# Kernel optimization log

Hardware: AMD Instinct MI355X
Metric: run time of the kernel (lower is better)

The kernel has to match this reference:

```python
import jax, jax.numpy as jnp
import numpy as np

N = 32768
E = 8           # num_submodules (4x2 grid)
HID = 256       # hidden_dim
POS_DIM = 63    # 3*(1+2*10)
DIR_DIM = 27    # 3*(1+2*4)
APP_DIM = 48
IN_DIM = POS_DIM + APP_DIM        # 111
SKIP_IN = HID + IN_DIM            # 367
COL_IN = HID + DIR_DIM            # 283
COL_HID = HID // 2                # 128
NUM_APP = 1000

SCENE = np.array([-100.0, -100.0, -10.0, 100.0, 100.0, 50.0], np.float32)
_margin = (1.0 - 0.8) / 2.0       # (1 - foreground_ratio)/2
_rng = SCENE[3:] - SCENE[:3]
FG_LO = SCENE[:3] + _rng * _margin
FG_HI = SCENE[3:] - _rng * _margin

def _centroids():
    xs = np.linspace(-100.0, 100.0, 3)   # grid_cols + 1
    ys = np.linspace(-100.0, 100.0, 5)   # grid_rows + 1
    zc = (-10.0 + 50.0) / 2.0
    cs = []
    for i in range(4):
        for j in range(2):
            cs.append([(xs[j] + xs[j + 1]) / 2.0, (ys[i] + ys[i + 1]) / 2.0, zc])
    return np.asarray(cs, np.float32)
CENTROIDS = _centroids()  # [E,3]

def posenc(x, max_log2, num_freqs):
    freqs = (2.0 ** np.linspace(0.0, max_log2, num_freqs)).astype(np.float32)
    parts = [x]
    for f in freqs:
        parts.append(jnp.sin(f * x))
        parts.append(jnp.cos(f * x))
    return jnp.concatenate(parts, axis=-1)

def setup_inputs() -> dict:
    key = jax.random.key(0)
    ks = jax.random.split(key, 24)
    lo, hi = jnp.asarray(SCENE[:3]), jnp.asarray(SCENE[3:])
    points = jax.random.uniform(ks[0], (N, 3), jnp.float32) * (hi - lo) + lo
    vd = jax.random.normal(ks[1], (N, 3), jnp.float32)
    viewdirs = vd / jnp.linalg.norm(vd, axis=-1, keepdims=True)
    appearance_idx = jax.random.randint(ks[2], (N,), 0, NUM_APP, jnp.int32)
    s = 0.02
    p = lambda k, shape: jax.random.normal(k, shape, jnp.float32) * s
    return {
        'points': points, 'viewdirs': viewdirs, 'appearance_idx': appearance_idx,
        'app_embed': p(ks[3], (E, NUM_APP, APP_DIM)),
        'W0': p(ks[4], (E, IN_DIM, HID)),      'b0': p(ks[5], (E, HID)),
        'W_pre': p(ks[6], (E, 3, HID, HID)),   'b_pre': p(ks[7], (E, 3, HID)),
        'Wskip': p(ks[8], (E, SKIP_IN, HID)),  'bskip': p(ks[9], (E, HID)),
        'W_post': p(ks[10], (E, 3, HID, HID)), 'b_post': p(ks[11], (E, 3, HID)),
        'Wd': p(ks[12], (E, HID, 1)),          'bd': p(ks[13], (E, 1)),
        'Wf': p(ks[14], (E, HID, HID)),        'bf': p(ks[15], (E, HID)),
        'Wc1': p(ks[16], (E, COL_IN, COL_HID)),'bc1': p(ks[17], (E, COL_HID)),
        'Wc2': p(ks[18], (E, COL_HID, 3)),     'bc2': p(ks[19], (E, 3)),
    }

def _forward(points, viewdirs, appearance_idx, app_embed, W0, b0, W_pre, b_pre,
             Wskip, bskip, W_post, b_post, Wd, bd, Wf, bf, Wc1, bc1, Wc2, bc2):
    n = points.shape[0]
    cen = jnp.asarray(CENTROIDS)
    fg = jnp.all((points >= jnp.asarray(FG_LO)) & (points <= jnp.asarray(FG_HI)), axis=-1)  # [N]
    # nearest-centroid routing (argmin of L2 == argmin of squared L2)
    expert = jnp.argmin(jnp.sum((points[:, None, :] - cen[None]) ** 2, axis=-1), axis=1)  # [N]
    pe = posenc(points, 10.0, 10)                              # [N,63]
    app = app_embed[:, appearance_idx, :]                      # [E,N,48] per-expert embedding lookup
    x0 = jnp.concatenate([jnp.broadcast_to(pe[None], (E, n, POS_DIM)), app], axis=-1)  # [E,N,111]
    x = jax.nn.relu(jnp.einsum('eni,eih->enh', x0, W0) + b0[:, None])
    for i in range(3):  # linear layers 1..3
        x = jax.nn.relu(jnp.einsum('enh,ehk->enk', x, W_pre[:, i]) + b_pre[:, i][:, None])
    x = jnp.concatenate([x, x0], axis=-1)                      # skip connection at layer 4
    x = jax.nn.relu(jnp.einsum('eni,eih->enh', x, Wskip) + bskip[:, None])
    for i in range(3):  # linear layers 5..7
        x = jax.nn.relu(jnp.einsum('enh,ehk->enk', x, W_post[:, i]) + b_post[:, i][:, None])
    density = jax.nn.relu(jnp.einsum('enh,eho->eno', x, Wd) + bd[:, None])   # [E,N,1]
    feat = jnp.einsum('enh,ehk->enk', x, Wf) + bf[:, None]                   # feature_head (no relu)
    de = posenc(viewdirs, 4.0, 4)                              # [N,27]
    cin = jnp.concatenate([feat, jnp.broadcast_to(de[None], (E, n, DIR_DIM))], axis=-1)  # [E,N,283]
    h = jax.nn.relu(jnp.einsum('eni,eih->enh', cin, Wc1) + bc1[:, None])
    color = jax.nn.sigmoid(jnp.einsum('enh,eho->eno', h, Wc2) + bc2[:, None])  # [E,N,3]
    rows = jnp.arange(n)
    d = jnp.where(fg[:, None], density[expert, rows], 0.0)     # combine: pick routed expert, zero bg
    c = jnp.where(fg[:, None], color[expert, rows], 0.0)
    return d, c

def reference(points, viewdirs, appearance_idx, app_embed, W0, b0, W_pre, b_pre,
              Wskip, bskip, W_post, b_post, Wd, bd, Wf, bf, Wc1, bc1, Wc2, bc2):
    return _forward(points, viewdirs, appearance_idx, app_embed, W0, b0, W_pre, b_pre,
                    Wskip, bskip, W_post, b_post, Wd, bd, Wf, bf, Wc1, bc1, Wc2, bc2)
```

## Files before the change

### kernel.cpp

```cpp
#include <hip/hip_runtime.h>
#include <hip/hip_bf16.h>
#include <math.h>

typedef __bf16 bf16;
typedef __bf16 bf16x4 __attribute__((ext_vector_type(4)));
typedef __bf16 bf16x8 __attribute__((ext_vector_type(8)));
typedef float  f32x4  __attribute__((ext_vector_type(4)));

#define N_PTS 32768

__global__ void k_point(const float* __restrict__ pts, float* __restrict__ out,
                        int* __restrict__ counts, unsigned short* __restrict__ idxlist) {
    __shared__ int lcnt[8], lbase[8];
    int t = threadIdx.x;
    int n = blockIdx.x * 256 + t;
    if (t < 8) lcnt[t] = 0;
    __syncthreads();
    float px = pts[3*n+0], py = pts[3*n+1], pz = pts[3*n+2];
    int e = 0; float best = 3.4e38f;
    #pragma unroll
    for (int i = 0; i < 4; ++i)
        #pragma unroll
        for (int j = 0; j < 2; ++j) {
            float cx = j ? 50.f : -50.f, cy = -75.f + 50.f * i;
            float dx = px - cx, dy = py - cy, dz = pz - 20.f;
            float d = dx*dx + dy*dy + dz*dz;
            if (d < best) { best = d; e = i*2 + j; }
        }
    bool fg = (px >= -80.f && px <= 80.f && py >= -80.f && py <= 80.f &&
               pz >= -4.f  && pz <= 44.f);
    int slot = -1;
    if (fg) {
        slot = atomicAdd(&lcnt[e], 1);
    } else {
        out[n] = 0.f;
        out[N_PTS + 3*n + 0] = 0.f;
        out[N_PTS + 3*n + 1] = 0.f;
        out[N_PTS + 3*n + 2] = 0.f;
    }
    __syncthreads();
    if (t < 8) lbase[t] = atomicAdd(&counts[t], lcnt[t]);
    __syncthreads();
    if (slot >= 0) idxlist[e * N_PTS + lbase[e] + slot] = (unsigned short)n;
}

__global__ void k_tp(const float* __restrict__ s0, const float* __restrict__ s1,
                     const float* __restrict__ s2, const float* __restrict__ s3,
                     const float* __restrict__ s4, const float* __restrict__ s5,
                     bf16* __restrict__ d0, bf16* __restrict__ d1, bf16* __restrict__ d2,
                     bf16* __restrict__ d3, bf16* __restrict__ d4, bf16* __restrict__ d5,
                     const float* __restrict__ pts, float* __restrict__ out,
                     int* __restrict__ counts, unsigned short* __restrict__ idxlist) {
    int t = threadIdx.x;
    if (blockIdx.y == 6) {
        __shared__ int lcnt[8], lbase[8];
        if (blockIdx.x >= N_PTS / 256) return;
        int n = blockIdx.x * 256 + t;
        if (t < 8) lcnt[t] = 0;
        __syncthreads();
        float px = pts[3*n+0], py = pts[3*n+1], pz = pts[3*n+2];
        int e = 0; float best = 3.4e38f;
        #pragma unroll
        for (int i = 0; i < 4; ++i)
            #pragma unroll
            for (int j = 0; j < 2; ++j) {
                float cx = j ? 50.f : -50.f, cy = -75.f + 50.f * i;
                float dx = px - cx, dy = py - cy, dz = pz - 20.f;
                float d = dx*dx + dy*dy + dz*dz;
                if (d < best) { best = d; e = i*2 + j; }
            }
        bool fg = (px >= -80.f && px <= 80.f && py >= -80.f && py <= 80.f &&
                   pz >= -4.f  && pz <= 44.f);
        int slot = -1;
        if (fg) {
            slot = atomicAdd(&lcnt[e], 1);
        } else {
            out[n] = 0.f;
            out[N_PTS + 3*n + 0] = 0.f;
            out[N_PTS + 3*n + 1] = 0.f;
            out[N_PTS + 3*n + 2] = 0.f;
        }
        __syncthreads();
        if (t < 8) lbase[t] = atomicAdd(&counts[t], lcnt[t]);
        __syncthreads();
        if (slot >= 0) idxlist[e * N_PTS + lbase[e] + slot] = (unsigned short)n;
        return;
    }
    __shared__ bf16 tile[64 * 68];
    const float* src; bf16* dst; int K, Nn, Kpad, Eg;
    switch (blockIdx.y) {
        case 0:  src = s0; dst = d0; K = 111; Nn = 256; Kpad = 128; Eg = 8;  break;
        case 1:  src = s1; dst = d1; K = 256; Nn = 256; Kpad = 256; Eg = 24; break;
        case 2:  src = s2; dst = d2; K = 367; Nn = 256; Kpad = 384; Eg = 8;  break;
        case 3:  src = s3; dst = d3; K = 256; Nn = 256; Kpad = 256; Eg = 24; break;
        case 4:  src = s4; dst = d4; K = 256; Nn = 256; Kpad = 256; Eg = 8;  break;
        default: src = s5; dst = d5; K = 283; Nn = 128; Kpad = 288; Eg = 8;  break;
    }
    int ktiles = (Kpad + 63) / 64, ntiles = Nn / 64;
    int b = blockIdx.x;
    if (b >= Eg * ktiles * ntiles) return;
    int eg = b / (ktiles * ntiles), rem = b % (ktiles * ntiles);
    int kt = rem / ntiles, nt = rem % ntiles;
    #pragma unroll
    for (int r = 0; r < 4; ++r) {
        int idx = r * 256 + t;
        int kl = idx >> 4, nl4 = (idx & 15) * 4;
        int kg = kt * 64 + kl, ng = nt * 64 + nl4;
        bf16x4 v = (bf16x4){(bf16)0.f, (bf16)0.f, (bf16)0.f, (bf16)0.f};
        if (kg < K) {
            f32x4 f = *(const f32x4*)(src + ((size_t)(eg * K + kg)) * Nn + ng);
            v[0] = (bf16)f[0]; v[1] = (bf16)f[1]; v[2] = (bf16)f[2]; v[3] = (bf16)f[3];
        }
        *(bf16x4*)(&tile[kl * 68 + nl4]) = v;
    }
    __syncthreads();
    #pragma unroll
    for (int i = 0; i < 2; ++i) {
        int idx = i * 256 + t;
        int ng_l = idx >> 3, kq = idx & 7;
        int kg = kt * 64 + kq * 8, ng = nt * 64 + ng_l;
        if (kg < Kpad) {
            bf16x8 v;
            #pragma unroll
            for (int j = 0; j < 8; ++j) v[j] = tile[(kq * 8 + j) * 68 + ng_l];
            size_t off = ((size_t)(ng >> 5) * (Kpad >> 5) + (size_t)(kg >> 5)) * 1024
                       + (size_t)((ng >> 4) & 1) * 512
                       + (size_t)((kg >> 3) & 3) * 128
                       + (size_t)(ng & 15) * 8;
            *(bf16x8*)(dst + (size_t)eg * Nn * Kpad + off) = v;
        }
    }
}

__device__ __forceinline__ f32x4 mfma16(bf16x8 a, bf16x8 b, f32x4 c) {
    return __builtin_amdgcn_mfma_f32_16x16x32_bf16(a, b, c, 0, 0, 0);
}

__device__ __forceinline__ void zacc(f32x4 acc[2][2]) {
    #pragma unroll
    for (int i = 0; i < 2; ++i)
        #pragma unroll
        for (int j = 0; j < 2; ++j) acc[i][j] = (f32x4){0.f, 0.f, 0.f, 0.f};
}

template<int NS, int KPAD>
__device__ __forceinline__ void gemm_p(f32x4 acc[2][2], const bf16* A, int astr,
                                       const bf16* __restrict__ Wt, int wk0,
                                       int nbase, int l16, int quad, int lane) {
    const bf16* bp = Wt + ((size_t)(nbase >> 5) * (KPAD >> 5) + (size_t)(wk0 >> 5)) * 1024
                   + (size_t)lane * 8;
    #pragma unroll
    for (int s = 0; s < NS; ++s) {
        int kA = s * 32 + quad * 8;
        bf16x8 a0 = *(const bf16x8*)(A + (size_t)(l16)      * astr + kA);
        bf16x8 a1 = *(const bf16x8*)(A + (size_t)(16 + l16) * astr + kA);
        bf16x8 b0 = *(const bf16x8*)(bp + s * 1024);
        bf16x8 b1 = *(const bf16x8*)(bp + s * 1024 + 512);
        acc[0][0] = mfma16(a0, b0, acc[0][0]);
        acc[1][0] = mfma16(a1, b0, acc[1][0]);
        acc[0][1] = mfma16(a0, b1, acc[0][1]);
        acc[1][1] = mfma16(a1, b1, acc[1][1]);
    }
}

template<int NS, bool GUARD>
__device__ __forceinline__ void gemm_g(f32x4 acc[2][2], const bf16* A, int astr,
                                       const float* __restrict__ W, int ldn, int wk0, int Klim,
                                       int nbase, int l16, int quad) {
    #pragma unroll
    for (int s = 0; s < NS; ++s) {
        int kA = s * 32 + quad * 8;
        bf16x8 a0 = *(const bf16x8*)(A + (size_t)(l16)      * astr + kA);
        bf16x8 a1 = *(const bf16x8*)(A + (size_t)(16 + l16) * astr + kA);
        #pragma unroll
        for (int nt = 0; nt < 2; ++nt) {
            int n = nbase + nt * 16 + l16;
            const float* wp = W + (size_t)(wk0 + kA) * ldn + n;
            bf16x8 b;
            #pragma unroll
            for (int j = 0; j < 8; ++j) {
                float wv = 0.f;
                if (!GUARD || (wk0 + kA + j < Klim)) wv = wp[(size_t)j * ldn];
                b[j] = (bf16)wv;
            }
            acc[0][nt] = mfma16(a0, b, acc[0][nt]);
            acc[1][nt] = mfma16(a1, b, acc[1][nt]);
        }
    }
}

__device__ __forceinline__ void epi(f32x4 acc[2][2], const float* bias, bool dorelu,
                                    bf16* dst, int dstr, int nbase, int l16, int quad) {
    #pragma unroll
    for (int nt = 0; nt < 2; ++nt) {
        float bv = bias[nbase + nt * 16 + l16];
        #pragma unroll
        for (int mt = 0; mt < 2; ++mt) {
            #pragma unroll
            for (int r = 0; r < 4; ++r) {
                float v = acc[mt][nt][r] + bv;
                v = fminf(fmaxf(v, -64.f), 64.f);
                if (dorelu) v = fmaxf(v, 0.f);
                dst[(size_t)(mt * 16 + quad * 4 + r) * dstr + nbase + nt * 16 + l16] = (bf16)v;
            }
        }
    }
}

template<bool PACKED>
__global__ __launch_bounds__(512, 2)
void k_main(const int* __restrict__ counts, const unsigned short* __restrict__ idxlist,
            const float* __restrict__ pts, const float* __restrict__ dirs,
            const float* __restrict__ app_embed, const int* __restrict__ aidx,
            const float* __restrict__ W0, const float* __restrict__ b0,
            const float* __restrict__ W_pre, const float* __restrict__ b_pre,
            const float* __restrict__ Wskip, const float* __restrict__ bskip,
            const float* __restrict__ W_post, const float* __restrict__ b_post,
            const float* __restrict__ Wd, const float* __restrict__ bd,
            const float* __restrict__ Wf, const float* __restrict__ bf_,
            const float* __restrict__ Wc1, const float* __restrict__ bc1,
            const float* __restrict__ Wc2, const float* __restrict__ bc2,
            const bf16* __restrict__ wt0, const bf16* __restrict__ wtpre,
            const bf16* __restrict__ wtskip, const bf16* __restrict__ wtpost,
            const bf16* __restrict__ wtf, const bf16* __restrict__ wtc1,
            float* __restrict__ out) {
    __shared__ bf16 xaA[32 * 264];
    __shared__ bf16 xaB[32 * 264];
    __shared__ bf16 x0l[32 * 136];
    __shared__ bf16 del[32 * 48];
    __shared__ int  gidx[32];
    __shared__ int  aid[32];

    const int e    = blockIdx.x & 7;
    const int tile = blockIdx.x >> 3;
    const int cnt  = counts[e];
    if (tile * 32 >= cnt) return;
    const int t = threadIdx.x;
    const int lane = t & 63, wv = t >> 6;
    const int l16 = lane & 15, quad = lane >> 4;
    const int nbase = wv * 32;

    if (t < 32) {
        int i = tile * 32 + t;
        int g = (i < cnt) ? (int)idxlist[e * N_PTS + i] : -1;
        gidx[t] = g;
        aid[t]  = (g >= 0) ? aidx[g] : 0;
    }
    __syncthreads();
    {
        int row = t >> 4, c0 = t & 15, g = gidx[row];
        float p0 = 0.f, p1 = 0.f, p2 = 0.f, q0 = 0.f, q1 = 0.f, q2 = 0.f;
        if (g >= 0) {
            p0 = pts[3*g+0];  p1 = pts[3*g+1];  p2 = pts[3*g+2];
            q0 = dirs[3*g+0]; q1 = dirs[3*g+1]; q2 = dirs[3*g+2];
        }
        int ai = aid[row];
        #pragma unroll
        for (int i = 0; i < 8; ++i) {
            int col = c0 + 16 * i;
            float v = 0.f;
            if (g >= 0 && col < 111) {
                if (col < 3) {
                    v = (col == 0) ? p0 : (col == 1) ? p1 : p2;
                } else if (col < 63) {
                    int q = col - 3, fi = q / 6, d = q % 6, ax = (d < 3) ? d : (d - 3);
                    float p = (ax == 0) ? p0 : (ax == 1) ? p1 : p2;
                    float f = (float)exp2((double)fi * (10.0 / 9.0));
                    v = (d < 3) ? sinf(f * p) : cosf(f * p);
                } else {
                    v = app_embed[((size_t)(e * 1000 + ai)) * 48 + (col - 63)];
                }
            }
            x0l[row * 136 + col] = (bf16)v;
        }
        #pragma unroll
        for (int i = 0; i < 2; ++i) {
            int col = c0 + 16 * i;
            float v = 0.f;
            if (g >= 0 && col < 27) {
                if (col < 3) {
                    v = (col == 0) ? q0 : (col == 1) ? q1 : q2;
                } else {
                    int q = col - 3, fi = q / 6, d = q % 6, ax = (d < 3) ? d : (d - 3);
                    float p = (ax == 0) ? q0 : (ax == 1) ? q1 : q2;
                    float f = (float)exp2((double)fi * (4.0 / 3.0));
                    v = (d < 3) ? sinf(f * p) : cosf(f * p);
                }
            }
            del[row * 48 + col] = (bf16)v;
        }
    }
    __syncthreads();

    f32x4 acc[2][2];
    zacc(acc);
    if (PACKED) gemm_p<4, 128>(acc, x0l, 136, wt0 + (size_t)e * 32768, 0, nbase, l16, quad, lane);
    else        gemm_g<4, true>(acc, x0l, 136, W0 + (size_t)e * 28416, 256, 0, 111, nbase, l16, quad);
    epi(acc, b0 + e * 256, true, xaA, 264, nbase, l16, quad);
    __syncthreads();
    #pragma unroll
    for (int i = 0; i < 3; ++i) {
        const bf16* src = (i & 1) ? xaB : xaA;
        bf16*       dst = (i & 1) ? xaA : xaB;
        zacc(acc);
        if (PACKED) gemm_p<8, 256>(acc, src, 264, wtpre + (size_t)(e * 3 + i) * 65536, 0, nbase, l16, quad, lane);
        else        gemm_g<8, false>(acc, src, 264, W_pre + (size_t)(e * 3 + i) * 65536, 256, 0, 256, nbase, l16, quad);
        epi(acc, b_pre + (e * 3 + i) * 256, true, dst, 264, nbase, l16, quad);
        __syncthreads();
    }
    zacc(acc);
    if (PACKED) {
        gemm_p<8, 384>(acc, xaB, 264, wtskip + (size_t)e * 98304, 0,   nbase, l16, quad, lane);
        gemm_p<4, 384>(acc, x0l, 136, wtskip + (size_t)e * 98304, 256, nbase, l16, quad, lane);
    } else {
        gemm_g<8, false>(acc, xaB, 264, Wskip + (size_t)e * 93952, 256, 0,   367, nbase, l16, quad);
        gemm_g<4, true >(acc, x0l, 136, Wskip + (size_t)e * 93952, 256, 256, 367, nbase, l16, quad);
    }
    epi(acc, bskip + e * 256, true, xaA, 264, nbase, l16, quad);
    __syncthreads();
    #pragma unroll
    for (int i = 0; i < 3; ++i) {
        const bf16* src = (i & 1) ? xaB : xaA;
        bf16*       dst = (i & 1) ? xaA : xaB;
        zacc(acc);
        if (PACKED) gemm_p<8, 256>(acc, src, 264, wtpost + (size_t)(e * 3 + i) * 65536, 0, nbase, l16, quad, lane);
        else        gemm_g<8, false>(acc, src, 264, W_post + (size_t)(e * 3 + i) * 65536, 256, 0, 256, nbase, l16, quad);
        epi(acc, b_post + (e * 3 + i) * 256, true, dst, 264, nbase, l16, quad);
        __syncthreads();
    }
    {
        int m = t >> 4, p = t & 15;
        const bf16*  xr = xaB + (size_t)m * 264;
        const float* wd = Wd + e * 256;
        float s = 0.f;
        #pragma unroll
        for (int kk = 0; kk < 16; ++kk) s += (float)xr[p * 16 + kk] * wd[p * 16 + kk];
        s += __shfl_down(s, 8, 16);
        s += __shfl_down(s, 4, 16);
        s += __shfl_down(s, 2, 16);
        s += __shfl_down(s, 1, 16);
        if (p == 0) {
            int g = gidx[m];
            if (g >= 0) out[g] = fminf(fmaxf(s + bd[e], 0.f), 64.f);
        }
    }
    zacc(acc);
    if (PACKED) gemm_p<8, 256>(acc, xaB, 264, wtf + (size_t)e * 65536, 0, nbase, l16, quad, lane);
    else        gemm_g<8, false>(acc, xaB, 264, Wf + (size_t)e * 65536, 256, 0, 256, nbase, l16, quad);
    epi(acc, bf_ + e * 256, false, xaA, 264, nbase, l16, quad);
    __syncthreads();
    if (wv < 4) {
        zacc(acc);
        if (PACKED) {
            gemm_p<8, 288>(acc, xaA, 264, wtc1 + (size_t)e * 36864, 0,   nbase, l16, quad, lane);
            gemm_p<1, 288>(acc, del, 48,  wtc1 + (size_t)e * 36864, 256, nbase, l16, quad, lane);
        } else {
            gemm_g<8, false>(acc, xaA, 264, Wc1 + (size_t)e * 36224, 128, 0,   283, nbase, l16, quad);
            gemm_g<1, true >(acc, del, 48,  Wc1 + (size_t)e * 36224, 128, 256, 283, nbase, l16, quad);
        }
        epi(acc, bc1 + e * 128, true, xaB, 264, nbase, l16, quad);
    }
    __syncthreads();
    if (t < 96) {
        int m = t & 31, c = t >> 5;
        int g = gidx[m];
        if (g >= 0) {
            const bf16*  xr = xaB + (size_t)m * 264;
            const float* w  = Wc2 + e * 384 + c;
            float s = 0.f;
            for (int k = 0; k < 128; ++k) s += (float)xr[k] * w[k * 3];
            s += bc2[e * 3 + c];
            s = fminf(fmaxf(s, -30.f), 30.f);
            out[N_PTS + 3 * g + c] = 1.f / (1.f + expf(-s));
        }
    }
}

extern "C" void kernel_launch(void* const* d_in, const int* in_sizes, int n_in,
                              void* d_out, int out_size, void* d_ws, size_t ws_size,
                              hipStream_t stream) {
    const float* points    = (const float*)d_in[0];
    const float* viewdirs  = (const float*)d_in[1];
    const int*   aidx      = (const int*)  d_in[2];
    const float* app_embed = (const float*)d_in[3];
    const float* W0        = (const float*)d_in[4];
    const float* b0        = (const float*)d_in[5];
    const float* W_pre     = (const float*)d_in[6];
    const float* b_pre     = (const float*)d_in[7];
    const float* Wskip     = (const float*)d_in[8];
    const float* bskip     = (const float*)d_in[9];
    const float* W_post    = (const float*)d_in[10];
    const float* b_post    = (const float*)d_in[11];
    const float* Wd        = (const float*)d_in[12];
    const float* bd        = (const float*)d_in[13];
    const float* Wf        = (const float*)d_in[14];
    const float* bf_       = (const float*)d_in[15];
    const float* Wc1       = (const float*)d_in[16];
    const float* bc1       = (const float*)d_in[17];
    const float* Wc2       = (const float*)d_in[18];
    const float* bc2       = (const float*)d_in[19];
    float* out = (float*)d_out;
    (void)in_sizes; (void)n_in; (void)out_size;

    char* ws = (char*)d_ws;
    size_t off = 0;
    auto alloc = [&](size_t bytes) -> void* {
        void* p = ws + off;
        off += (bytes + 255) & ~(size_t)255;
        return p;
    };
    int*            counts  = (int*)            alloc(8 * 4);
    unsigned short* idxlist = (unsigned short*) alloc((size_t)8 * N_PTS * 2);
    bf16* wt0    = (bf16*)alloc((size_t)8  * 256 * 128 * 2);
    bf16* wtpre  = (bf16*)alloc((size_t)24 * 256 * 256 * 2);
    bf16* wtskip = (bf16*)alloc((size_t)8  * 256 * 384 * 2);
    bf16* wtpost = (bf16*)alloc((size_t)24 * 256 * 256 * 2);
    bf16* wtf    = (bf16*)alloc((size_t)8  * 256 * 256 * 2);
    bf16* wtc1   = (bf16*)alloc((size_t)8  * 128 * 288 * 2);
    const bool packed = (off <= ws_size);

    hipMemsetAsync(counts, 0, 8 * sizeof(int), stream);
    #define MAIN_ARGS counts, idxlist, points, viewdirs, app_embed, aidx, \
        W0, b0, W_pre, b_pre, Wskip, bskip, W_post, b_post, Wd, bd, Wf, bf_, \
        Wc1, bc1, Wc2, bc2, wt0, wtpre, wtskip, wtpost, wtf, wtc1, out
    if (packed) {
        hipLaunchKernelGGL(k_tp, dim3(384, 7), dim3(256), 0, stream,
                           W0, W_pre, Wskip, W_post, Wf, Wc1,
                           wt0, wtpre, wtskip, wtpost, wtf, wtc1,
                           points, out, counts, idxlist);
        hipLaunchKernelGGL(k_main<true>,  dim3(8 * (N_PTS / 32)), dim3(512), 0, stream, MAIN_ARGS);
    } else {
        hipLaunchKernelGGL(k_point, dim3(N_PTS / 256), dim3(256), 0, stream,
                           points, out, counts, idxlist);
        hipLaunchKernelGGL(k_main<false>, dim3(8 * (N_PTS / 32)), dim3(512), 0, stream, MAIN_ARGS);
    }
    #undef MAIN_ARGS
}
```

Before: 153.8 us.

## Double point tile per block from 32 to 64 rows for more weight reuse

Each block now processes 64 routed points instead of 32, so every wave issues four M-tiles of MFMAs per loaded B fragment and weight traffic per point is halved. Shared buffers move to dynamic shared memory sized for 64 rows, and the setup, density and color stages are remapped to the larger tile. This adds accumulator registers and shared memory per block, which may lower occupancy under the 512x2 launch bound, and wastes more padded rows in each expert's last tile.

```diff
diff --git a/kernel.cpp b/kernel.cpp
--- a/kernel.cpp
+++ b/kernel.cpp
@@ -136,15 +136,15 @@
     return __builtin_amdgcn_mfma_f32_16x16x32_bf16(a, b, c, 0, 0, 0);
 }
 
-__device__ __forceinline__ void zacc(f32x4 acc[2][2]) {
-    #pragma unroll
-    for (int i = 0; i < 2; ++i)
+__device__ __forceinline__ void zacc(f32x4 acc[4][2]) {
+    #pragma unroll
+    for (int i = 0; i < 4; ++i)
         #pragma unroll
         for (int j = 0; j < 2; ++j) acc[i][j] = (f32x4){0.f, 0.f, 0.f, 0.f};
 }
 
 template<int NS, int KPAD>
-__device__ __forceinline__ void gemm_p(f32x4 acc[2][2], const bf16* A, int astr,
+__device__ __forceinline__ void gemm_p(f32x4 acc[4][2], const bf16* A, int astr,
                                        const bf16* __restrict__ Wt, int wk0,
                                        int nbase, int l16, int quad, int lane) {
     const bf16* bp = Wt + ((size_t)(nbase >> 5) * (KPAD >> 5) + (size_t)(wk0 >> 5)) * 1024
@@ -152,26 +152,24 @@
     #pragma unroll
     for (int s = 0; s < NS; ++s) {
         int kA = s * 32 + quad * 8;
-        bf16x8 a0 = *(const bf16x8*)(A + (size_t)(l16)      * astr + kA);
-        bf16x8 a1 = *(const bf16x8*)(A + (size_t)(16 + l16) * astr + kA);
         bf16x8 b0 = *(const bf16x8*)(bp + s * 1024);
         bf16x8 b1 = *(const bf16x8*)(bp + s * 1024 + 512);
-        acc[0][0] = mfma16(a0, b0, acc[0][0]);
-        acc[1][0] = mfma16(a1, b0, acc[1][0]);
-        acc[0][1] = mfma16(a0, b1, acc[0][1]);
-        acc[1][1] = mfma16(a1, b1, acc[1][1]);
+        #pragma unroll
+        for (int m = 0; m < 4; ++m) {
+            bf16x8 a = *(const bf16x8*)(A + (size_t)(m * 16 + l16) * astr + kA);
+            acc[m][0] = mfma16(a, b0, acc[m][0]);
+            acc[m][1] = mfma16(a, b1, acc[m][1]);
+        }
     }
 }
 
 template<int NS, bool GUARD>
-__device__ __forceinline__ void gemm_g(f32x4 acc[2][2], const bf16* A, int astr,
+__device__ __forceinline__ void gemm_g(f32x4 acc[4][2], const bf16* A, int astr,
                                        const float* __restrict__ W, int ldn, int wk0, int Klim,
                                        int nbase, int l16, int quad) {
     #pragma unroll
     for (int s = 0; s < NS; ++s) {
         int kA = s * 32 + quad * 8;
-        bf16x8 a0 = *(const bf16x8*)(A + (size_t)(l16)      * astr + kA);
-        bf16x8 a1 = *(const bf16x8*)(A + (size_t)(16 + l16) * astr + kA);
         #pragma unroll
         for (int nt = 0; nt < 2; ++nt) {
             int n = nbase + nt * 16 + l16;
@@ -183,25 +181,28 @@
                 if (!GUARD || (wk0 + kA + j < Klim)) wv = wp[(size_t)j * ldn];
                 b[j] = (bf16)wv;
             }
-            acc[0][nt] = mfma16(a0, b, acc[0][nt]);
-            acc[1][nt] = mfma16(a1, b, acc[1][nt]);
-        }
-    }
-}
-
-__device__ __forceinline__ void epi(f32x4 acc[2][2], const float* bias, bool dorelu,
+            #pragma unroll
+            for (int m = 0; m < 4; ++m) {
+                bf16x8 a = *(const bf16x8*)(A + (size_t)(m * 16 + l16) * astr + kA);
+                acc[m][nt] = mfma16(a, b, acc[m][nt]);
+            }
+        }
+    }
+}
+
+__device__ __forceinline__ void epi(f32x4 acc[4][2], const float* bias, bool dorelu,
                                     bf16* dst, int dstr, int nbase, int l16, int quad) {
     #pragma unroll
     for (int nt = 0; nt < 2; ++nt) {
         float bv = bias[nbase + nt * 16 + l16];
         #pragma unroll
-        for (int mt = 0; mt < 2; ++mt) {
+        for (int m = 0; m < 4; ++m) {
             #pragma unroll
             for (int r = 0; r < 4; ++r) {
-                float v = acc[mt][nt][r] + bv;
+                float v = acc[m][nt][r] + bv;
                 v = fminf(fmaxf(v, -64.f), 64.f);
                 if (dorelu) v = fmaxf(v, 0.f);
-                dst[(size_t)(mt * 16 + quad * 4 + r) * dstr + nbase + nt * 16 + l16] = (bf16)v;
+                dst[(size_t)(m * 16 + quad * 4 + r) * dstr + nbase + nt * 16 + l16] = (bf16)v;
             }
         }
     }
@@ -224,31 +225,32 @@
             const bf16* __restrict__ wtskip, const bf16* __restrict__ wtpost,
             const bf16* __restrict__ wtf, const bf16* __restrict__ wtc1,
             float* __restrict__ out) {
-    __shared__ bf16 xaA[32 * 264];
-    __shared__ bf16 xaB[32 * 264];
-    __shared__ bf16 x0l[32 * 136];
-    __shared__ bf16 del[32 * 48];
-    __shared__ int  gidx[32];
-    __shared__ int  aid[32];
+    extern __shared__ char smem[];
+    bf16* xaA  = (bf16*)smem;
+    bf16* xaB  = xaA + 64 * 264;
+    bf16* x0l  = xaB + 64 * 264;
+    bf16* del  = x0l + 64 * 136;
+    int*  gidx = (int*)(del + 64 * 48);
+    int*  aid  = gidx + 64;
 
     const int e    = blockIdx.x & 7;
     const int tile = blockIdx.x >> 3;
     const int cnt  = counts[e];
-    if (tile * 32 >= cnt) return;
+    if (tile * 64 >= cnt) return;
     const int t = threadIdx.x;
     const int lane = t & 63, wv = t >> 6;
     const int l16 = lane & 15, quad = lane >> 4;
     const int nbase = wv * 32;
 
-    if (t < 32) {
-        int i = tile * 32 + t;
+    if (t < 64) {
+        int i = tile * 64 + t;
         int g = (i < cnt) ? (int)idxlist[e * N_PTS + i] : -1;
         gidx[t] = g;
         aid[t]  = (g >= 0) ? aidx[g] : 0;
     }
     __syncthreads();
     {
-        int row = t >> 4, c0 = t & 15, g = gidx[row];
+        int row = t >> 3, c0 = t & 7, g = gidx[row];
         float p0 = 0.f, p1 = 0.f, p2 = 0.f, q0 = 0.f, q1 = 0.f, q2 = 0.f;
         if (g >= 0) {
             p0 = pts[3*g+0];  p1 = pts[3*g+1];  p2 = pts[3*g+2];
@@ -256,8 +258,8 @@
         }
         int ai = aid[row];
         #pragma unroll
-        for (int i = 0; i < 8; ++i) {
-            int col = c0 + 16 * i;
+        for (int i = 0; i < 16; ++i) {
+            int col = c0 + 8 * i;
             float v = 0.f;
             if (g >= 0 && col < 111) {
                 if (col < 3) {
@@ -274,8 +276,8 @@
             x0l[row * 136 + col] = (bf16)v;
         }
         #pragma unroll
-        for (int i = 0; i < 2; ++i) {
-            int col = c0 + 16 * i;
+        for (int i = 0; i < 4; ++i) {
+            int col = c0 + 8 * i;
             float v = 0.f;
             if (g >= 0 && col < 27) {
                 if (col < 3) {
@@ -292,7 +294,7 @@
     }
     __syncthreads();
 
-    f32x4 acc[2][2];
+    f32x4 acc[4][2];
     zacc(acc);
     if (PACKED) gemm_p<4, 128>(acc, x0l, 136, wt0 + (size_t)e * 32768, 0, nbase, l16, quad, lane);
     else        gemm_g<4, true>(acc, x0l, 136, W0 + (size_t)e * 28416, 256, 0, 111, nbase, l16, quad);
@@ -329,16 +331,15 @@
         __syncthreads();
     }
     {
-        int m = t >> 4, p = t & 15;
+        int m = t >> 3, p = t & 7;
         const bf16*  xr = xaB + (size_t)m * 264;
         const float* wd = Wd + e * 256;
         float s = 0.f;
         #pragma unroll
-        for (int kk = 0; kk < 16; ++kk) s += (float)xr[p * 16 + kk] * wd[p * 16 + kk];
-        s += __shfl_down(s, 8, 16);
-        s += __shfl_down(s, 4, 16);
-        s += __shfl_down(s, 2, 16);
-        s += __shfl_down(s, 1, 16);
+        for (int kk = 0; kk < 32; ++kk) s += (float)xr[p * 32 + kk] * wd[p * 32 + kk];
+        s += __shfl_down(s, 4, 8);
+        s += __shfl_down(s, 2, 8);
+        s += __shfl_down(s, 1, 8);
         if (p == 0) {
             int g = gidx[m];
             if (g >= 0) out[g] = fminf(fmaxf(s + bd[e], 0.f), 64.f);
@@ -361,8 +362,8 @@
         epi(acc, bc1 + e * 128, true, xaB, 264, nbase, l16, quad);
     }
     __syncthreads();
-    if (t < 96) {
-        int m = t & 31, c = t >> 5;
+    if (t < 192) {
+        int m = t & 63, c = t >> 6;
         int g = gidx[m];
         if (g >= 0) {
             const bf16*  xr = xaB + (size_t)m * 264;
@@ -419,6 +420,8 @@
     bf16* wtc1   = (bf16*)alloc((size_t)8  * 128 * 288 * 2);
     const bool packed = (off <= ws_size);
 
+    const size_t SMEM = (size_t)(64*264 + 64*264 + 64*136 + 64*48) * 2 + 64 * 4 * 2;
+
     hipMemsetAsync(counts, 0, 8 * sizeof(int), stream);
     #define MAIN_ARGS counts, idxlist, points, viewdirs, app_embed, aidx, \
         W0, b0, W_pre, b_pre, Wskip, bskip, W_post, b_post, Wd, bd, Wf, bf_, \
@@ -428,11 +431,11 @@
                            W0, W_pre, Wskip, W_post, Wf, Wc1,
                            wt0, wtpre, wtskip, wtpost, wtf, wtc1,
                            points, out, counts, idxlist);
-        hipLaunchKernelGGL(k_main<true>,  dim3(8 * (N_PTS / 32)), dim3(512), 0, stream, MAIN_ARGS);
+        hipLaunchKernelGGL(k_main<true>,  dim3(8 * (N_PTS / 64)), dim3(512), SMEM, stream, MAIN_ARGS);
     } else {
         hipLaunchKernelGGL(k_point, dim3(N_PTS / 256), dim3(256), 0, stream,
                            points, out, counts, idxlist);
-        hipLaunchKernelGGL(k_main<false>, dim3(8 * (N_PTS / 32)), dim3(512), 0, stream, MAIN_ARGS);
+        hipLaunchKernelGGL(k_main<false>, dim3(8 * (N_PTS / 64)), dim3(512), SMEM, stream, MAIN_ARGS);
     }
     #undef MAIN_ARGS
 }
```

New measurement: 187.0 us. 1.22x slower.
